# Performance work log

Hardware: AMD Instinct MI355X
Metric: run time of the kernel (lower is better)

The kernel has to match this reference:

```python
import jax, jax.numpy as jnp
import numpy as np

NUM_NODES = 50000
NUM_EDGES = 600000
IN_DIM = 128
HID = 128
OUT_DIM = 10
NUM_GRAPHS = 64


def setup_inputs() -> dict:
    key = jax.random.key(0)
    ks = jax.random.split(key, 12)
    x = jax.random.normal(ks[0], (NUM_NODES, IN_DIM), dtype=jnp.float32)
    edge_index = jax.random.randint(ks[1], (2, NUM_EDGES), 0, NUM_NODES, dtype=jnp.int64)
    batch = jnp.sort(jax.random.randint(ks[2], (NUM_NODES,), 0, NUM_GRAPHS, dtype=jnp.int64))
    s = 0.05
    W1 = jax.random.normal(ks[3], (IN_DIM, HID), dtype=jnp.float32) * s
    b1 = jnp.zeros((HID,), dtype=jnp.float32)
    W2 = jax.random.normal(ks[4], (HID, HID), dtype=jnp.float32) * s
    b2 = jnp.zeros((HID,), dtype=jnp.float32)
    W3 = jax.random.normal(ks[5], (HID, HID), dtype=jnp.float32) * s
    b3 = jnp.zeros((HID,), dtype=jnp.float32)
    Wlin = jax.random.normal(ks[6], (HID, OUT_DIM), dtype=jnp.float32) * s
    blin = jnp.zeros((OUT_DIM,), dtype=jnp.float32)
    return {"x": x, "edge_index": edge_index, "batch": batch,
            "W1": W1, "b1": b1, "W2": W2, "b2": b2, "W3": W3, "b3": b3,
            "Wlin": Wlin, "blin": blin}


def _gcn_conv(x, W, b, src, dst, norm):
    # h = X W ; out[i] = sum_{(j->i)} norm_e * h[j] ; + bias
    h = x @ W                                   # [N, H]
    msg = h[src] * norm[:, None]                # [E+N, H] gather + scale
    out = jax.ops.segment_sum(msg, dst, num_segments=x.shape[0])  # scatter-add
    return out + b


def reference(x, edge_index, batch, W1, b1, W2, b2, W3, b3, Wlin, blin):
    N = x.shape[0]
    # add self loops (PyG GCNConv default)
    loops = jnp.arange(N, dtype=edge_index.dtype)
    src = jnp.concatenate([edge_index[0], loops])
    dst = jnp.concatenate([edge_index[1], loops])
    # symmetric normalization D^{-1/2} (A+I) D^{-1/2}; degree on target nodes
    deg = jax.ops.segment_sum(jnp.ones_like(dst, dtype=x.dtype), dst, num_segments=N)
    dinv = jnp.where(deg > 0, jax.lax.rsqrt(deg), 0.0)
    norm = dinv[src] * dinv[dst]

    h = jax.nn.relu(_gcn_conv(x, W1, b1, src, dst, norm))   # dropout = identity (eval)
    h = jax.nn.relu(_gcn_conv(h, W2, b2, src, dst, norm))
    h = jax.nn.relu(_gcn_conv(h, W3, b3, src, dst, norm))

    # global mean pool over graphs
    sums = jax.ops.segment_sum(h, batch, num_segments=NUM_GRAPHS)          # [G, H]
    cnts = jax.ops.segment_sum(jnp.ones((N,), dtype=h.dtype), batch, num_segments=NUM_GRAPHS)
    pooled = sums / jnp.maximum(cnts, 1.0)[:, None]
    return pooled @ Wlin + blin                                            # [G, OUT]
```

## Files before the change

kernel.cpp:

```cpp
#include <hip/hip_runtime.h>
#include <hip/hip_bf16.h>
#include <hip/hip_fp16.h>


#define HID 128
#define NGRAPH 64

typedef _Float16 half8v __attribute__((ext_vector_type(8)));
typedef float floatx4 __attribute__((ext_vector_type(4)));

__device__ __forceinline__ int idx_at(const void* p, long long i, int f64) {
    if (f64) return (int)((const long long*)p)[i];
    return ((const int*)p)[i];
}

__global__ void init_kernel(const int* __restrict__ ei, int* __restrict__ flag,
                            int* __restrict__ counts, float* __restrict__ pooled,
                            float* __restrict__ gcnt, int N) {
    int i = blockIdx.x * blockDim.x + threadIdx.x;
    if (i < N) counts[i] = 0;
    if (i < NGRAPH * HID) pooled[i] = 0.f;
    if (i < NGRAPH) gcnt[i] = 0.f;
    if (blockIdx.x == 0) {
        __shared__ int cnt;
        if (threadIdx.x == 0) cnt = 0;
        __syncthreads();
        int z = 0;
        for (int k = threadIdx.x; k < 2048; k += 256)
            if (ei[2 * k + 1] == 0) z++;
        atomicAdd(&cnt, z);
        __syncthreads();
        if (threadIdx.x == 0) *flag = (cnt > 1024) ? 1 : 0;
    }
}

__global__ void hist_kernel(const void* __restrict__ ei, const int* __restrict__ flag,
                            int* __restrict__ counts, int E, int N) {
    int e = blockIdx.x * blockDim.x + threadIdx.x;
    if (e >= E) return;
    int f64 = *flag;
    int d = idx_at(ei, (long long)E + e, f64);
    if ((unsigned)d < (unsigned)N) atomicAdd(&counts[d], 1);
}

__device__ __forceinline__ int wave_incl_scan(int v, int lane) {
#pragma unroll
    for (int off = 1; off < 64; off <<= 1) {
        int u = __shfl_up(v, off);
        if (lane >= off) v += u;
    }
    return v;
}

__global__ __launch_bounds__(256) void blocksum_kernel(const int* __restrict__ counts,
                                                       int* __restrict__ bsums, int N) {
    int i = blockIdx.x * 256 + threadIdx.x;
    int v = (i < N) ? counts[i] : 0;
    int lane = threadIdx.x & 63, w = threadIdx.x >> 6;
#pragma unroll
    for (int off = 32; off > 0; off >>= 1) v += __shfl_down(v, off);
    __shared__ int ws[4];
    if (lane == 0) ws[w] = v;
    __syncthreads();
    if (threadIdx.x == 0) bsums[blockIdx.x] = ws[0] + ws[1] + ws[2] + ws[3];
}

__global__ __launch_bounds__(256) void scanb_kernel(int* __restrict__ bsums, int nb) {
    int t = threadIdx.x;
    int lane = t & 63, w = t >> 6;
    int v = (t < nb) ? bsums[t] : 0;
    int iv = wave_incl_scan(v, lane);
    __shared__ int wsum[4];
    if (lane == 63) wsum[w] = iv;
    __syncthreads();
    int add = 0;
    for (int k = 0; k < w; ++k) add += wsum[k];
    if (t < nb) bsums[t] = iv - v + add;
}

__global__ __launch_bounds__(256) void fill_kernel(const int* __restrict__ counts,
                                                   const int* __restrict__ bsums,
                                                   int* __restrict__ rowstart,
                                                   int* __restrict__ cursor,
                                                   float* __restrict__ dinv, int N) {
    int i = blockIdx.x * 256 + threadIdx.x;
    int c = (i < N) ? counts[i] : 0;
    int lane = threadIdx.x & 63, w = threadIdx.x >> 6;
    int iv = wave_incl_scan(c, lane);
    __shared__ int wsum[4];
    if (lane == 63) wsum[w] = iv;
    __syncthreads();
    int add = bsums[blockIdx.x];
    for (int k = 0; k < w; ++k) add += wsum[k];
    int excl = iv - c + add;
    if (i < N) {
        rowstart[i] = excl;
        cursor[i] = excl;
        dinv[i] = rsqrtf((float)(c + 1));
        if (i == N - 1) rowstart[N] = excl + c;
    }
}

__global__ void scatter_kernel(const void* __restrict__ ei, const int* __restrict__ flag,
                               int* __restrict__ cursor,
                               unsigned short* __restrict__ csr_src, int E, int N) {
    int e = blockIdx.x * blockDim.x + threadIdx.x;
    if (e >= E) return;
    int f64 = *flag;
    int s = idx_at(ei, e, f64);
    int d = idx_at(ei, (long long)E + e, f64);
    if ((unsigned)s >= (unsigned)N || (unsigned)d >= (unsigned)N) return;
    int pos = atomicAdd(&cursor[d], 1);
    csr_src[pos] = (unsigned short)s;
}

__global__ __launch_bounds__(256) void prep_kernel(const float* __restrict__ x,
                                                   const float* __restrict__ dinv,
                                                   __half2* __restrict__ xs,
                                                   const float* __restrict__ W1,
                                                   const float* __restrict__ W2,
                                                   const float* __restrict__ W3,
                                                   half8v* __restrict__ wf, int n2) {
    if (blockIdx.x < 24) {
        int which = blockIdx.x >> 3;
        const float* W = which == 0 ? W1 : (which == 1 ? W2 : W3);
        int t = (blockIdx.x & 7) * 256 + threadIdx.x;
        int lane = t & 63;
        int nt = (t >> 6) & 7;
        int kblk = t >> 9;
        int n = nt * 16 + (lane & 15);
        int kbase = kblk * 32 + (lane >> 4) * 8;
        half8v v;
#pragma unroll
        for (int j = 0; j < 8; ++j) v[j] = (_Float16)W[(size_t)(kbase + j) * 128 + n];
        wf[which * 2048 + t] = v;
    } else {
        int i = (blockIdx.x - 24) * 256 + threadIdx.x;
        if (i >= n2) return;
        float dv = dinv[i >> 6];
        float2 v = ((const float2*)x)[i];
        xs[i] = __floats2half2_rn(dv * v.x, dv * v.y);
    }
}

__global__ __launch_bounds__(256) void agg_kernel(const __half2* __restrict__ xs,
                                                  const int* __restrict__ rowstart,
                                                  const unsigned short* __restrict__ csr_src,
                                                  const float* __restrict__ dinv,
                                                  __half2* __restrict__ out, int N) {
    int wid = (blockIdx.x * blockDim.x + threadIdx.x) >> 6;
    int lane = threadIdx.x & 63;
    if (wid >= N) return;
    float di = dinv[wid];
    float2 s0 = __half22float2(xs[(size_t)wid * 64 + lane]);
    float accx = s0.x, accy = s0.y;
    float bccx = 0.f, bccy = 0.f;
    int e0 = rowstart[wid], e1 = rowstart[wid + 1];
    int e = e0;
    for (; e + 8 <= e1; e += 8) {
        int s[8]; __half2 v[8];
#pragma unroll
        for (int u = 0; u < 8; ++u) s[u] = csr_src[e + u];
#pragma unroll
        for (int u = 0; u < 8; ++u) v[u] = xs[(size_t)s[u] * 64 + lane];
#pragma unroll
        for (int u = 0; u < 8; u += 2) {
            float2 f0 = __half22float2(v[u]);
            float2 f1 = __half22float2(v[u + 1]);
            accx += f0.x; accy += f0.y;
            bccx += f1.x; bccy += f1.y;
        }
    }
    for (; e + 4 <= e1; e += 4) {
        int s[4]; __half2 v[4];
#pragma unroll
        for (int u = 0; u < 4; ++u) s[u] = csr_src[e + u];
#pragma unroll
        for (int u = 0; u < 4; ++u) v[u] = xs[(size_t)s[u] * 64 + lane];
#pragma unroll
        for (int u = 0; u < 4; u += 2) {
            float2 f0 = __half22float2(v[u]);
            float2 f1 = __half22float2(v[u + 1]);
            accx += f0.x; accy += f0.y;
            bccx += f1.x; bccy += f1.y;
        }
    }
    for (; e < e1; ++e) {
        int s = csr_src[e];
        float2 f = __half22float2(xs[(size_t)s * 64 + lane]);
        accx += f.x; accy += f.y;
    }
    out[(size_t)wid * 64 + lane] = __floats2half2_rn(di * (accx + bccx),
                                                     di * (accy + bccy));
}

template <bool SCALED>
__global__ __launch_bounds__(256) void gemm_mfma(const __half2* __restrict__ A16,
                                                 const half8v* __restrict__ wf,
                                                 const float* __restrict__ bias,
                                                 const float* __restrict__ dinv,
                                                 __half2* __restrict__ O16, int M) {
    int wid = threadIdx.x >> 6, lane = threadIdx.x & 63;
    int rowTile = blockIdx.x * 64 + wid * 16;
    int hi = lane >> 4;
    int arow = rowTile + (lane & 15);
    if (arow >= M) arow = M - 1;
    const half8v* Arow = (const half8v*)((const _Float16*)A16 + (size_t)arow * 128);

    floatx4 acc[8];
#pragma unroll
    for (int nt = 0; nt < 8; ++nt) acc[nt] = (floatx4){0.f, 0.f, 0.f, 0.f};

#pragma unroll
    for (int kb = 0; kb < 4; ++kb) {
        half8v a = Arow[kb * 4 + hi];
#pragma unroll
        for (int nt = 0; nt < 8; ++nt) {
            half8v w = wf[(kb * 8 + nt) * 64 + lane];
            acc[nt] = __builtin_amdgcn_mfma_f32_16x16x32_f16(a, w, acc[nt], 0, 0, 0);
        }
    }

    int ocol_lo = lane & 15;
    int orow0 = rowTile + hi * 4;
    float dv[4];
#pragma unroll
    for (int r = 0; r < 4; ++r) {
        int orow = orow0 + r;
        dv[r] = (SCALED && orow < M) ? dinv[orow] : 1.0f;
    }
#pragma unroll
    for (int nt = 0; nt < 8; ++nt) {
        int col = nt * 16 + ocol_lo;
        float b = bias[col];
#pragma unroll
        for (int r = 0; r < 4; ++r) {
            int orow = orow0 + r;
            if (orow < M) {
                float v = fmaxf(acc[nt][r] + b, 0.f);
                if (SCALED) v *= dv[r];
                ((_Float16*)O16)[(size_t)orow * 128 + col] = (_Float16)v;
            }
        }
    }
}

#define POOL_CHUNK 16
__global__ __launch_bounds__(256) void pool_kernel(const __half2* __restrict__ h,
                                                   const void* __restrict__ batch,
                                                   const int* __restrict__ flag,
                                                   float* __restrict__ pooled,
                                                   float* __restrict__ gcnt, int N) {
    int wid = (blockIdx.x * blockDim.x + threadIdx.x) >> 6;
    int lane = threadIdx.x & 63;
    int n0 = wid * POOL_CHUNK;
    if (n0 >= N) return;
    int n1 = n0 + POOL_CHUNK; if (n1 > N) n1 = N;
    int f64 = *flag;
    int g = idx_at(batch, n0, f64);
    float ax = 0.f, ay = 0.f;
    int cnt = 0;
    for (int n = n0; n < n1; ++n) {
        int gn = idx_at(batch, n, f64);
        if (gn != g) {
            if ((unsigned)g < (unsigned)NGRAPH) {
                atomicAdd(&pooled[g * HID + 2 * lane], ax);
                atomicAdd(&pooled[g * HID + 2 * lane + 1], ay);
                if (lane == 0) atomicAdd(&gcnt[g], (float)cnt);
            }
            ax = ay = 0.f; cnt = 0; g = gn;
        }
        float2 v = __half22float2(h[(size_t)n * 64 + lane]);
        ax += v.x; ay += v.y; cnt++;
    }
    if ((unsigned)g < (unsigned)NGRAPH) {
        atomicAdd(&pooled[g * HID + 2 * lane], ax);
        atomicAdd(&pooled[g * HID + 2 * lane + 1], ay);
        if (lane == 0) atomicAdd(&gcnt[g], (float)cnt);
    }
}

__global__ __launch_bounds__(128) void final_kernel(const float* __restrict__ pooled,
                                                    const float* __restrict__ gcnt,
                                                    const float* __restrict__ Wl,
                                                    const float* __restrict__ bl,
                                                    float* __restrict__ out) {
    int o = blockIdx.x * blockDim.x + threadIdx.x;
    if (o >= NGRAPH * 10) return;
    int g = o / 10, c = o % 10;
    float inv = 1.0f / fmaxf(gcnt[g], 1.0f);
    float acc = 0.f;
    for (int k = 0; k < HID; ++k)
        acc = fmaf(pooled[g * HID + k], Wl[k * 10 + c], acc);
    out[o] = acc * inv + bl[c];
}

extern "C" void kernel_launch(void* const* d_in, const int* in_sizes, int n_in,
                              void* d_out, int out_size, void* d_ws, size_t ws_size,
                              hipStream_t stream) {
    const float* x   = (const float*)d_in[0];
    const void* ei   = d_in[1];
    const void* bat  = d_in[2];
    const float* W1  = (const float*)d_in[3];
    const float* b1  = (const float*)d_in[4];
    const float* W2  = (const float*)d_in[5];
    const float* b2  = (const float*)d_in[6];
    const float* W3  = (const float*)d_in[7];
    const float* b3  = (const float*)d_in[8];
    const float* Wl  = (const float*)d_in[9];
    const float* bl  = (const float*)d_in[10];
    float* out = (float*)d_out;

    const int N = in_sizes[0] / HID;
    const int E = in_sizes[1] / 2;

    char* w = (char*)d_ws;
    size_t off = 0;
    auto carve = [&](size_t bytes) -> void* {
        void* p = w + off;
        off = (off + bytes + 255) & ~(size_t)255;
        return p;
    };
    __half2* xs       = (__half2*)carve((size_t)N * HID * 2);
    __half2* aggB16   = (__half2*)carve((size_t)N * HID * 2);
    __half2* hsA      = (__half2*)carve((size_t)N * HID * 2);
    __half2* hsB      = (__half2*)carve((size_t)N * HID * 2);
    int*     counts   = (int*)carve((size_t)N * 4);
    int*     rowstart = (int*)carve((size_t)(N + 1) * 4);
    int*     cursor   = (int*)carve((size_t)N * 4);
    float*   dinv     = (float*)carve((size_t)N * 4);
    unsigned short* csr_src = (unsigned short*)carve((size_t)E * 2);
    float*   pooled   = (float*)carve((size_t)NGRAPH * HID * 4);
    float*   gcnt     = (float*)carve((size_t)NGRAPH * 4);
    half8v*  wf       = (half8v*)carve(3 * 2048 * 16);
    int*     bsums    = (int*)carve(1024);
    int*     flag     = (int*)carve(256);

    const int nb = (N + 255) / 256;
    const int n2 = N * HID / 2;

    init_kernel<<<nb, 256, 0, stream>>>((const int*)ei, flag, counts, pooled, gcnt, N);
    hist_kernel<<<(E + 255) / 256, 256, 0, stream>>>(ei, flag, counts, E, N);
    blocksum_kernel<<<nb, 256, 0, stream>>>(counts, bsums, N);
    scanb_kernel<<<1, 256, 0, stream>>>(bsums, nb);
    fill_kernel<<<nb, 256, 0, stream>>>(counts, bsums, rowstart, cursor, dinv, N);
    scatter_kernel<<<(E + 255) / 256, 256, 0, stream>>>(ei, flag, cursor, csr_src, E, N);
    prep_kernel<<<24 + (n2 + 255) / 256, 256, 0, stream>>>(x, dinv, xs,
                                                           W1, W2, W3, wf, n2);

    int aggBlocks  = (N + 3) / 4;
    int gemmBlocks = (N + 63) / 64;

    agg_kernel<<<aggBlocks, 256, 0, stream>>>(xs, rowstart, csr_src, dinv, aggB16, N);
    gemm_mfma<true><<<gemmBlocks, 256, 0, stream>>>(aggB16, wf, b1, dinv, hsA, N);
    agg_kernel<<<aggBlocks, 256, 0, stream>>>(hsA, rowstart, csr_src, dinv, aggB16, N);
    gemm_mfma<true><<<gemmBlocks, 256, 0, stream>>>(aggB16, wf + 2048, b2, dinv, hsB, N);
    agg_kernel<<<aggBlocks, 256, 0, stream>>>(hsB, rowstart, csr_src, dinv, aggB16, N);
    gemm_mfma<false><<<gemmBlocks, 256, 0, stream>>>(aggB16, wf + 4096, b3, dinv, hsA, N);

    int poolWaves = (N + POOL_CHUNK - 1) / POOL_CHUNK;
    int poolBlocks = (poolWaves + 3) / 4;
    pool_kernel<<<poolBlocks, 256, 0, stream>>>(hsA, bat, flag, pooled, gcnt, N);
    final_kernel<<<5, 128, 0, stream>>>(pooled, gcnt, Wl, bl, out);
}
```

Before: 240.9 us.

## Pad CSR rows to multiples of eight with a zero sentinel node

```diff
diff --git a/kernel.cpp b/kernel.cpp
--- a/kernel.cpp
+++ b/kernel.cpp
@@ -16,11 +16,16 @@
 
 __global__ void init_kernel(const int* __restrict__ ei, int* __restrict__ flag,
                             int* __restrict__ counts, float* __restrict__ pooled,
-                            float* __restrict__ gcnt, int N) {
+                            float* __restrict__ gcnt, uint4* __restrict__ csr4,
+                            int N, int nCsr4) {
     int i = blockIdx.x * blockDim.x + threadIdx.x;
+    int stride = gridDim.x * blockDim.x;
     if (i < N) counts[i] = 0;
     if (i < NGRAPH * HID) pooled[i] = 0.f;
     if (i < NGRAPH) gcnt[i] = 0.f;
+    unsigned fillv = (unsigned)N | ((unsigned)N << 16);
+    uint4 fv = make_uint4(fillv, fillv, fillv, fillv);
+    for (int j = i; j < nCsr4; j += stride) csr4[j] = fv;
     if (blockIdx.x == 0) {
         __shared__ int cnt;
         if (threadIdx.x == 0) cnt = 0;
@@ -55,7 +60,7 @@
 __global__ __launch_bounds__(256) void blocksum_kernel(const int* __restrict__ counts,
                                                        int* __restrict__ bsums, int N) {
     int i = blockIdx.x * 256 + threadIdx.x;
-    int v = (i < N) ? counts[i] : 0;
+    int v = (i < N) ? ((counts[i] + 7) & ~7) : 0;
     int lane = threadIdx.x & 63, w = threadIdx.x >> 6;
 #pragma unroll
     for (int off = 32; off > 0; off >>= 1) v += __shfl_down(v, off);
@@ -85,19 +90,20 @@
                                                    float* __restrict__ dinv, int N) {
     int i = blockIdx.x * 256 + threadIdx.x;
     int c = (i < N) ? counts[i] : 0;
+    int cp = (c + 7) & ~7;
     int lane = threadIdx.x & 63, w = threadIdx.x >> 6;
-    int iv = wave_incl_scan(c, lane);
+    int iv = wave_incl_scan(cp, lane);
     __shared__ int wsum[4];
     if (lane == 63) wsum[w] = iv;
     __syncthreads();
     int add = bsums[blockIdx.x];
     for (int k = 0; k < w; ++k) add += wsum[k];
-    int excl = iv - c + add;
+    int excl = iv - cp + add;
     if (i < N) {
         rowstart[i] = excl;
         cursor[i] = excl;
         dinv[i] = rsqrtf((float)(c + 1));
-        if (i == N - 1) rowstart[N] = excl + c;
+        if (i == N - 1) rowstart[N] = excl + cp;
     }
 }
 
@@ -117,10 +123,13 @@
 __global__ __launch_bounds__(256) void prep_kernel(const float* __restrict__ x,
                                                    const float* __restrict__ dinv,
                                                    __half2* __restrict__ xs,
+                                                   __half2* __restrict__ hsA,
+                                                   __half2* __restrict__ hsB,
                                                    const float* __restrict__ W1,
                                                    const float* __restrict__ W2,
                                                    const float* __restrict__ W3,
-                                                   half8v* __restrict__ wf, int n2) {
+                                                   half8v* __restrict__ wf,
+                                                   int N, int n2) {
     if (blockIdx.x < 24) {
         int which = blockIdx.x >> 3;
         const float* W = which == 0 ? W1 : (which == 1 ? W2 : W3);
@@ -134,8 +143,14 @@
 #pragma unroll
         for (int j = 0; j < 8; ++j) v[j] = (_Float16)W[(size_t)(kbase + j) * 128 + n];
         wf[which * 2048 + t] = v;
+    } else if (blockIdx.x == 24) {
+        int t = threadIdx.x;
+        __half2 z = __floats2half2_rn(0.f, 0.f);
+        if (t < 64) xs[(size_t)N * 64 + t] = z;
+        else if (t < 128) hsA[(size_t)N * 64 + (t - 64)] = z;
+        else if (t < 192) hsB[(size_t)N * 64 + (t - 128)] = z;
     } else {
-        int i = (blockIdx.x - 24) * 256 + threadIdx.x;
+        int i = (blockIdx.x - 25) * 256 + threadIdx.x;
         if (i >= n2) return;
         float dv = dinv[i >> 6];
         float2 v = ((const float2*)x)[i];
@@ -156,39 +171,28 @@
     float accx = s0.x, accy = s0.y;
     float bccx = 0.f, bccy = 0.f;
     int e0 = rowstart[wid], e1 = rowstart[wid + 1];
-    int e = e0;
-    for (; e + 8 <= e1; e += 8) {
-        int s[8]; __half2 v[8];
-#pragma unroll
-        for (int u = 0; u < 8; ++u) s[u] = csr_src[e + u];
-#pragma unroll
-        for (int u = 0; u < 8; ++u) v[u] = xs[(size_t)s[u] * 64 + lane];
-#pragma unroll
-        for (int u = 0; u < 8; u += 2) {
-            float2 f0 = __half22float2(v[u]);
-            float2 f1 = __half22float2(v[u + 1]);
-            accx += f0.x; accy += f0.y;
-            bccx += f1.x; bccy += f1.y;
-        }
-    }
-    for (; e + 4 <= e1; e += 4) {
-        int s[4]; __half2 v[4];
-#pragma unroll
-        for (int u = 0; u < 4; ++u) s[u] = csr_src[e + u];
-#pragma unroll
-        for (int u = 0; u < 4; ++u) v[u] = xs[(size_t)s[u] * 64 + lane];
-#pragma unroll
-        for (int u = 0; u < 4; u += 2) {
-            float2 f0 = __half22float2(v[u]);
-            float2 f1 = __half22float2(v[u + 1]);
-            accx += f0.x; accy += f0.y;
-            bccx += f1.x; bccy += f1.y;
-        }
-    }
-    for (; e < e1; ++e) {
-        int s = csr_src[e];
-        float2 f = __half22float2(xs[(size_t)s * 64 + lane]);
-        accx += f.x; accy += f.y;
+    for (int e = e0; e < e1; e += 8) {
+        uint4 q = *(const uint4*)(csr_src + e);
+        int s0i = q.x & 0xffff, s1i = q.x >> 16;
+        int s2i = q.y & 0xffff, s3i = q.y >> 16;
+        int s4i = q.z & 0xffff, s5i = q.z >> 16;
+        int s6i = q.w & 0xffff, s7i = q.w >> 16;
+        __half2 v0 = xs[(size_t)s0i * 64 + lane];
+        __half2 v1 = xs[(size_t)s1i * 64 + lane];
+        __half2 v2 = xs[(size_t)s2i * 64 + lane];
+        __half2 v3 = xs[(size_t)s3i * 64 + lane];
+        __half2 v4 = xs[(size_t)s4i * 64 + lane];
+        __half2 v5 = xs[(size_t)s5i * 64 + lane];
+        __half2 v6 = xs[(size_t)s6i * 64 + lane];
+        __half2 v7 = xs[(size_t)s7i * 64 + lane];
+        float2 f0 = __half22float2(v0), f1 = __half22float2(v1);
+        float2 f2 = __half22float2(v2), f3 = __half22float2(v3);
+        float2 f4 = __half22float2(v4), f5 = __half22float2(v5);
+        float2 f6 = __half22float2(v6), f7 = __half22float2(v7);
+        accx += f0.x + f2.x; accy += f0.y + f2.y;
+        bccx += f1.x + f3.x; bccy += f1.y + f3.y;
+        accx += f4.x + f6.x; accy += f4.y + f6.y;
+        bccx += f5.x + f7.x; bccy += f5.y + f7.y;
     }
     out[(size_t)wid * 64 + lane] = __floats2half2_rn(di * (accx + bccx),
                                                      di * (accy + bccy));
@@ -313,6 +317,7 @@
 
     const int N = in_sizes[0] / HID;
     const int E = in_sizes[1] / 2;
+    const int EPAD = (E + 7 * N + 7) & ~7;
 
     char* w = (char*)d_ws;
     size_t off = 0;
@@ -321,15 +326,15 @@
         off = (off + bytes + 255) & ~(size_t)255;
         return p;
     };
-    __half2* xs       = (__half2*)carve((size_t)N * HID * 2);
+    __half2* xs       = (__half2*)carve((size_t)(N + 1) * HID * 2);
     __half2* aggB16   = (__half2*)carve((size_t)N * HID * 2);
-    __half2* hsA      = (__half2*)carve((size_t)N * HID * 2);
-    __half2* hsB      = (__half2*)carve((size_t)N * HID * 2);
+    __half2* hsA      = (__half2*)carve((size_t)(N + 1) * HID * 2);
+    __half2* hsB      = (__half2*)carve((size_t)(N + 1) * HID * 2);
     int*     counts   = (int*)carve((size_t)N * 4);
     int*     rowstart = (int*)carve((size_t)(N + 1) * 4);
     int*     cursor   = (int*)carve((size_t)N * 4);
     float*   dinv     = (float*)carve((size_t)N * 4);
-    unsigned short* csr_src = (unsigned short*)carve((size_t)E * 2);
+    unsigned short* csr_src = (unsigned short*)carve((size_t)EPAD * 2);
     float*   pooled   = (float*)carve((size_t)NGRAPH * HID * 4);
     float*   gcnt     = (float*)carve((size_t)NGRAPH * 4);
     half8v*  wf       = (half8v*)carve(3 * 2048 * 16);
@@ -339,14 +344,15 @@
     const int nb = (N + 255) / 256;
     const int n2 = N * HID / 2;
 
-    init_kernel<<<nb, 256, 0, stream>>>((const int*)ei, flag, counts, pooled, gcnt, N);
+    init_kernel<<<nb, 256, 0, stream>>>((const int*)ei, flag, counts, pooled, gcnt,
+                                        (uint4*)csr_src, N, EPAD / 8);
     hist_kernel<<<(E + 255) / 256, 256, 0, stream>>>(ei, flag, counts, E, N);
     blocksum_kernel<<<nb, 256, 0, stream>>>(counts, bsums, N);
     scanb_kernel<<<1, 256, 0, stream>>>(bsums, nb);
     fill_kernel<<<nb, 256, 0, stream>>>(counts, bsums, rowstart, cursor, dinv, N);
     scatter_kernel<<<(E + 255) / 256, 256, 0, stream>>>(ei, flag, cursor, csr_src, E, N);
-    prep_kernel<<<24 + (n2 + 255) / 256, 256, 0, stream>>>(x, dinv, xs,
-                                                           W1, W2, W3, wf, n2);
+    prep_kernel<<<25 + (n2 + 255) / 256, 256, 0, stream>>>(x, dinv, xs, hsA, hsB,
+                                                           W1, W2, W3, wf, N, n2);
 
     int aggBlocks  = (N + 3) / 4;
     int gemmBlocks = (N + 63) / 64;
```

Measured after the change: 230.4 us. 1.05x faster.
